# Kernel tuning notes

Hardware: AMD Instinct MI355X
Metric: run time of the kernel (lower is better)

## Reference

```python
import jax, jax.numpy as jnp
import numpy as np
from math import factorial, sqrt

L_MAX = 3
MUL = 64
# e3nn FullyConnectedTensorProduct instruction order: lexicographic over (l1, l2, l3)
# keeping paths with triangle inequality and matching parity ((-1)^(l1+l2) == (-1)^l3).
PATHS = [(l1, l2, l3)
         for l1 in range(L_MAX + 1)
         for l2 in range(L_MAX + 1)
         for l3 in range(L_MAX + 1)
         if abs(l1 - l2) <= l3 <= l1 + l2 and (l1 + l2 + l3) % 2 == 0]
assert len(PATHS) == 23
N_TO = {l3: sum(1 for p in PATHS if p[2] == l3) for l3 in range(L_MAX + 1)}


def _su2_cg(j1, m1, j2, m2, j3, m3):
    # Complex-basis Clebsch-Gordan coefficient (Racah formula), as in e3nn.
    if m3 != m1 + m2:
        return 0.0
    f = factorial
    vmin = max(-j1 + j2 + m3, -j1 + m1, 0)
    vmax = min(j2 + j3 + m1, j3 - j1 + j2, j3 + m3)
    c = sqrt((2 * j3 + 1) * f(j3 + j1 - j2) * f(j3 - j1 + j2) * f(j1 + j2 - j3)
             * f(j3 + m3) * f(j3 - m3)
             / (f(j1 + j2 + j3 + 1) * f(j1 - m1) * f(j1 + m1) * f(j2 - m2) * f(j2 + m2)))
    s = 0.0
    for v in range(vmin, vmax + 1):
        s += (-1) ** (v + j2 + m2) / f(v) * f(j2 + j3 + m1 - v) * f(j1 - m1 + v) \
             / f(j3 - j1 + j2 - v) / f(j3 + m3 - v) / f(v + j1 - j2 - m3)
    return c * s


def _q(l):
    # Change of basis real -> complex spherical harmonics (e3nn convention).
    q = np.zeros((2 * l + 1, 2 * l + 1), dtype=np.complex128)
    for m in range(-l, 0):
        q[l + m, l + abs(m)] = 1.0 / np.sqrt(2.0)
        q[l + m, l - abs(m)] = -1j / np.sqrt(2.0)
    q[l, l] = 1.0
    for m in range(1, l + 1):
        q[l + m, l + abs(m)] = (-1) ** m / np.sqrt(2.0)
        q[l + m, l - abs(m)] = 1j * (-1) ** m / np.sqrt(2.0)
    return (-1j) ** l * q


def _w3j(l1, l2, l3):
    # Real-basis Wigner 3j tensor, unit Frobenius norm (e3nn's o3.wigner_3j).
    csu2 = np.zeros((2 * l1 + 1, 2 * l2 + 1, 2 * l3 + 1))
    for m1 in range(-l1, l1 + 1):
        for m2 in range(-l2, l2 + 1):
            m3 = m1 + m2
            if -l3 <= m3 <= l3:
                csu2[l1 + m1, l2 + m2, l3 + m3] = _su2_cg(l1, m1, l2, m2, l3, m3)
    q1, q2, q3 = _q(l1), _q(l2), _q(l3)
    c = np.einsum('ij,kl,mn,ikn->jlm', q1, q2, np.conj(q3.T), csu2.astype(np.complex128))
    c = np.real(c)
    return (c / np.linalg.norm(c)).astype(np.float32)


W3J = {p: jnp.asarray(_w3j(*p)) for p in PATHS}
# e3nn 'component' irrep_normalization + 'element' path_normalization:
# per-path coeff = sqrt(ir_out.dim / (n_paths_into_out * mul1 * mul2)).
COEFF = {p: float(np.sqrt((2 * p[2] + 1) / (N_TO[p[2]] * MUL * MUL))) for p in PATHS}


def setup_inputs():
    key = jax.random.key(0)
    kx, kw = jax.random.split(key)
    x = jax.random.normal(kx, (2, 1024, MUL * (L_MAX + 1) ** 2), dtype=jnp.float32)
    weights = jax.random.normal(kw, (len(PATHS), MUL, MUL, MUL), dtype=jnp.float32)
    return {"x": x, "weights": weights}


def reference(x, weights):
    B, N, D = x.shape
    Z = B * N
    xf = x.reshape(Z, D)
    # e3nn layout: blocks of (mul, 2l+1) concatenated over l; offset = MUL * l^2.
    xs = [xf[:, MUL * l * l: MUL * (l + 1) ** 2].reshape(Z, MUL, 2 * l + 1)
          for l in range(L_MAX + 1)]
    acc = [jnp.zeros((Z, MUL, 2 * l + 1), dtype=x.dtype) for l in range(L_MAX + 1)]
    for p, (l1, l2, l3) in enumerate(PATHS):
        c = W3J[(l1, l2, l3)]
        t1 = jnp.einsum('zui,ijk->zujk', xs[l1], c)            # [Z,u,2l2+1,2l3+1]
        t2 = jnp.einsum('zujk,zvj->zuvk', t1, xs[l2])          # [Z,u,v,2l3+1]
        seg = jnp.einsum('zuvk,uvw->zwk', t2, weights[p]) * COEFF[(l1, l2, l3)]
        acc[l3] = acc[l3] + seg
    out = jnp.concatenate([a.reshape(Z, -1) for a in acc], axis=-1)
    return out.reshape(B, N, -1)
```

## Files before the change

kernel.cpp:

```cpp
#include <hip/hip_runtime.h>

struct CD { double re, im; };
constexpr CD cmul(CD a, CD b){ return CD{a.re*b.re - a.im*b.im, a.re*b.im + a.im*b.re}; }
constexpr CD conj_(CD a){ return CD{a.re, -a.im}; }

constexpr double factd(int n){ double r = 1.0; for(int i = 2; i <= n; ++i) r *= (double)i; return r; }
constexpr double csqrt_(double x){
  if (x <= 0.0) return 0.0;
  double g = x > 1.0 ? x : 1.0;
  for (int i = 0; i < 100; ++i) g = 0.5*(g + x/g);
  return g;
}

constexpr double su2_cg(int j1,int m1,int j2,int m2,int j3,int m3){
  if (m3 != m1 + m2) return 0.0;
  int vmin = -j1 + j2 + m3;
  if (-j1 + m1 > vmin) vmin = -j1 + m1;
  if (0 > vmin) vmin = 0;
  int vmax = j2 + j3 + m1;
  if (j3 - j1 + j2 < vmax) vmax = j3 - j1 + j2;
  if (j3 + m3 < vmax) vmax = j3 + m3;
  double c = csqrt_((2.0*j3 + 1.0) * factd(j3 + j1 - j2) * factd(j3 - j1 + j2) * factd(j1 + j2 - j3)
                    * factd(j3 + m3) * factd(j3 - m3)
                    / (factd(j1 + j2 + j3 + 1) * factd(j1 - m1) * factd(j1 + m1)
                       * factd(j2 - m2) * factd(j2 + m2)));
  double s = 0.0;
  for (int v = vmin; v <= vmax; ++v){
    double t = (((v + j2 + m2) & 1) ? -1.0 : 1.0) / factd(v)
               * factd(j2 + j3 + m1 - v) * factd(j1 - m1 + v)
               / factd(j3 - j1 + j2 - v) / factd(j3 + m3 - v) / factd(v + j1 - j2 - m3);
    s += t;
  }
  return c * s;
}

struct QM { CD m[7][7]; };
constexpr QM qmat(int l){
  QM q{};
  double is2 = 1.0 / csqrt_(2.0);
  for (int mm = -l; mm < 0; ++mm){
    q.m[l+mm][l-mm] = CD{is2, 0.0};
    q.m[l+mm][l+mm] = CD{0.0, -is2};
  }
  q.m[l][l] = CD{1.0, 0.0};
  for (int mm = 1; mm <= l; ++mm){
    double sgn = (mm & 1) ? -1.0 : 1.0;
    q.m[l+mm][l+mm] = CD{sgn*is2, 0.0};
    q.m[l+mm][l-mm] = CD{0.0, sgn*is2};
  }
  CD ph = (l % 4 == 0) ? CD{1,0} : (l % 4 == 1) ? CD{0,-1} : (l % 4 == 2) ? CD{-1,0} : CD{0,1};
  for (int r = 0; r < 7; ++r)
    for (int c = 0; c < 7; ++c)
      q.m[r][c] = cmul(ph, q.m[r][c]);
  return q;
}

template<int L1,int L2,int L3> struct W3JT { float v[2*L1+1][2*L2+1][2*L3+1]; };

template<int L1,int L2,int L3>
constexpr W3JT<L1,L2,L3> make_w3j(){
  constexpr int D1 = 2*L1+1, D2 = 2*L2+1, D3 = 2*L3+1;
  QM q1 = qmat(L1), q2 = qmat(L2), q3 = qmat(L3);
  double cg[7][7] = {};
  for (int i = 0; i < D1; ++i)
    for (int k = 0; k < D2; ++k){
      int n = i + k - L1 - L2 + L3;
      if (n >= 0 && n < D3) cg[i][k] = su2_cg(L1, i-L1, L2, k-L2, L3, (i-L1)+(k-L2));
    }
  double c[D1][D2][D3] = {};
  double norm2 = 0.0;
  for (int j = 0; j < D1; ++j)
    for (int l = 0; l < D2; ++l)
      for (int m = 0; m < D3; ++m){
        CD s{0.0, 0.0};
        for (int i = 0; i < D1; ++i)
          for (int k = 0; k < D2; ++k){
            double g = cg[i][k];
            if (g == 0.0) continue;
            int n = i + k - L1 - L2 + L3;
            CD t = cmul(q1.m[i][j], q2.m[k][l]);
            t = cmul(t, conj_(q3.m[n][m]));
            s.re += t.re * g; s.im += t.im * g;
          }
        c[j][l][m] = s.re;
        norm2 += s.re * s.re;
      }
  double inv = 1.0 / csqrt_(norm2);
  W3JT<L1,L2,L3> w{};
  for (int j = 0; j < D1; ++j)
    for (int l = 0; l < D2; ++l)
      for (int m = 0; m < D3; ++m){
        double val = c[j][l][m] * inv;
        if (val < 1e-10 && val > -1e-10) val = 0.0;
        w.v[j][l][m] = (float)val;
      }
  return w;
}

__device__ __constant__ int L3P_[23]  = {0,1,2,3,1,0,2,1,3,2,2,1,3,0,2,1,3,3,2,1,3,0,2};
__device__ __constant__ int SWAPP_[23] = {0,1,1,1,0,0,0,1,1,1,0,0,0,0,0,1,1,0,0,0,0,0,0};
constexpr int K3CUM[24] = {0,1,4,9,16,19,20,25,28,35,40,45,48,55,56,61,64,71,78,83,86,93,94,99};
constexpr size_t PSLICE = 2048ull * 64ull;

typedef __bf16 bf16x8 __attribute__((ext_vector_type(8)));
typedef float  f32x4  __attribute__((ext_vector_type(4)));
typedef float  f32x2  __attribute__((ext_vector_type(2)));

__global__ void pack_w_kernel(const float* __restrict__ w, unsigned short* __restrict__ wp, int total){
  int idx = blockIdx.x * 256 + threadIdx.x;
  if (idx >= total) return;
  int e    = idx & 7;
  int lane = (idx >> 3) & 63;
  int nt   = (idx >> 9) & 3;
  int hf   = (idx >> 11) & 1;
  int s    = (idx >> 12) & 63;
  int p    = idx >> 18;
  int kv = hf*32 + (lane >> 4)*8 + e;
  int wc = nt*16 + (lane & 15);
  int l3 = L3P_[p];
  const float nto[4] = {4.f, 6.f, 7.f, 6.f};
  float coeff = sqrtf((2.f*l3 + 1.f) / (nto[l3] * 4096.f));
  int a = SWAPP_[p] ? kv : s;
  int b = SWAPP_[p] ? s : kv;
  float val = w[(((size_t)p*64 + a)*64 + b)*64 + wc] * coeff;
  unsigned bits = __builtin_bit_cast(unsigned, val);
  unsigned r = (bits + 0x7FFFu + ((bits >> 16) & 1u)) >> 16;
  wp[idx] = (unsigned short)r;
}

__global__ void transpose_x(const float* __restrict__ x, float* __restrict__ xT){
  __shared__ float t[32][33];
  int bx = blockIdx.x, by = blockIdx.y;
  int tx = threadIdx.x & 31, ty = threadIdx.x >> 5;
  #pragma unroll
  for (int r = 0; r < 4; ++r)
    t[ty + r*8][tx] = x[(size_t)(by*32 + ty + r*8)*1024 + bx*32 + tx];
  __syncthreads();
  #pragma unroll
  for (int r = 0; r < 4; ++r)
    xT[(size_t)(bx*32 + ty + r*8)*2048 + by*32 + tx] = t[tx][ty + r*8];
}

template<int P,int L1,int L2,int L3,bool SWAP,int G0,int G,bool PART>
__device__ __forceinline__ void run_slot(
    int tile, const float* __restrict__ xT,
    const unsigned short* __restrict__ wp,
    float* __restrict__ dst, float* lds)
{
  constexpr int K3 = 2*L3+1;
  constexpr int LK = SWAP ? L1 : L2;
  constexpr int LS = SWAP ? L2 : L1;
  constexpr int DK = 2*LK+1, DS = 2*LS+1;
  constexpr auto C = make_w3j<L1,L2,L3>();

  const int lane = threadIdx.x & 63;
  const int wv   = threadIdx.x >> 6;
  const int zc   = tile*16 + (lane & 15);
  float* red = lds;
  float* tl  = lds + 3072 + wv*1040;

  f32x2 xk2[4][DK];
  {
    const float* xkb = xT + (size_t)(64*LK*LK)*2048 + zc;
    const int t0 = wv*32 + (lane >> 4)*8;
    #pragma unroll
    for (int q = 0; q < 4; ++q)
      #pragma unroll
      for (int t = 0; t < DK; ++t){
        float lo = xkb[(size_t)((t0 + 2*q    )*DK + t)*2048];
        float hi = xkb[(size_t)((t0 + 2*q + 1)*DK + t)*2048];
        xk2[q][t] = f32x2{lo, hi};
      }
  }

  const float* xsp = xT + (size_t)(64*LS*LS)*2048 + zc;
  const unsigned short* wu = wp + (size_t)P*262144 + (size_t)wv*2048 + (size_t)lane*8;

  f32x4 acc[G][4];
  #pragma unroll
  for (int a = 0; a < G; ++a)
    #pragma unroll
    for (int b = 0; b < 4; ++b) acc[a][b] = f32x4{0.f,0.f,0.f,0.f};

  float xs[DS];
  #pragma unroll
  for (int j = 0; j < DS; ++j) xs[j] = xsp[(size_t)j*2048];

  for (int s = 0; s < 64; ++s){
    bf16x8 bfrag[4];
    #pragma unroll
    for (int nt = 0; nt < 4; ++nt)
      bfrag[nt] = *reinterpret_cast<const bf16x8*>(wu + nt*512);

    const float* xnp = (s < 63) ? xsp + (size_t)DS*2048 : xsp;
    float xn[DS];
    #pragma unroll
    for (int j = 0; j < DS; ++j) xn[j] = xnp[(size_t)j*2048];

    #pragma unroll
    for (int kk = 0; kk < G; ++kk){
      float dk[DK];
      #pragma unroll
      for (int t = 0; t < DK; ++t) dk[t] = 0.f;
      #pragma unroll
      for (int t = 0; t < DK; ++t){
        #pragma unroll
        for (int j = 0; j < DS; ++j){
          const float cv = SWAP ? C.v[t][j][G0+kk] : C.v[j][t][G0+kk];
          if (cv != 0.0f) dk[t] = __builtin_fmaf(xs[j], cv, dk[t]);
        }
      }
      f32x2 af2[4];
      #pragma unroll
      for (int q = 0; q < 4; ++q) af2[q] = f32x2{0.f, 0.f};
      #pragma unroll
      for (int t = 0; t < DK; ++t){
        const f32x2 d2 = f32x2{dk[t], dk[t]};
        #pragma unroll
        for (int q = 0; q < 4; ++q)
          af2[q] += xk2[q][t] * d2;
      }
      bf16x8 af;
      #pragma unroll
      for (int q = 0; q < 4; ++q){
        af[2*q]   = (__bf16)af2[q].x;
        af[2*q+1] = (__bf16)af2[q].y;
      }
      __builtin_amdgcn_s_setprio(1);
      #pragma unroll
      for (int nt = 0; nt < 4; ++nt)
        acc[kk][nt] = __builtin_amdgcn_mfma_f32_16x16x32_bf16(af, bfrag[nt], acc[kk][nt], 0, 0, 0);
      __builtin_amdgcn_s_setprio(0);
    }
    #pragma unroll
    for (int j = 0; j < DS; ++j) xs[j] = xn[j];
    xsp += (size_t)DS*2048;
    wu  += 4096;
  }

  constexpr int Gh = (G + 1) / 2;
  static_assert(Gh <= 3, "red[] sized for Gh<=3");
  auto store_kk = [&](int kk, const f32x4 (&sum)[4]){
    if constexpr (PART){
      #pragma unroll
      for (int nt = 0; nt < 4; ++nt)
        #pragma unroll
        for (int r = 0; r < 4; ++r)
          tl[(((lane >> 4)*4 + r))*65 + nt*16 + (lane & 15)] = sum[nt][r];
      #pragma unroll
      for (int zr = 0; zr < 16; ++zr){
        float v = tl[zr*65 + lane];
        dst[(size_t)K3CUM[P]*PSLICE + ((size_t)(tile*16 + zr)*K3 + (G0+kk))*64 + lane] = v;
      }
    } else {
      #pragma unroll
      for (int nt = 0; nt < 4; ++nt)
        #pragma unroll
        for (int r = 0; r < 4; ++r){
          int zl = ((lane >> 4) << 2) + r;
          int wc = nt*16 + (lane & 15);
          unsafeAtomicAdd(dst + (size_t)(tile*16 + zl)*1024 + 64*L3*L3 + wc*K3 + (G0+kk),
                          sum[nt][r]);
        }
    }
  };

  if (wv == 1){
    #pragma unroll
    for (int kk = 0; kk < Gh; ++kk)
      #pragma unroll
      for (int nt = 0; nt < 4; ++nt)
        *reinterpret_cast<f32x4*>(&red[((kk*4 + nt)*64 + lane)*4]) = acc[kk][nt];
  }
  __syncthreads();
  if (wv == 0){
    #pragma unroll
    for (int kk = 0; kk < Gh; ++kk){
      f32x4 sum[4];
      #pragma unroll
      for (int nt = 0; nt < 4; ++nt){
        f32x4 o = *reinterpret_cast<const f32x4*>(&red[((kk*4 + nt)*64 + lane)*4]);
        sum[nt] = acc[kk][nt] + o;
      }
      store_kk(kk, sum);
    }
  }
  if constexpr (G > Gh){
    if (wv == 0){
      #pragma unroll
      for (int kk = Gh; kk < G; ++kk)
        #pragma unroll
        for (int nt = 0; nt < 4; ++nt)
          *reinterpret_cast<f32x4*>(&red[(((kk-Gh)*4 + nt)*64 + lane)*4]) = acc[kk][nt];
    }
    __syncthreads();
    if (wv == 1){
      #pragma unroll
      for (int kk = Gh; kk < G; ++kk){
        f32x4 sum[4];
        #pragma unroll
        for (int nt = 0; nt < 4; ++nt){
          f32x4 o = *reinterpret_cast<const f32x4*>(&red[(((kk-Gh)*4 + nt)*64 + lane)*4]);
          sum[nt] = acc[kk][nt] + o;
        }
        store_kk(kk, sum);
      }
    }
  }
}

template<bool PART>
__global__ __launch_bounds__(128, 3) void tp_main(const float* __restrict__ xT,
    const unsigned short* __restrict__ wp, float* __restrict__ dst)
{
  __shared__ __align__(16) float lds[5152];
  const int slot = blockIdx.x >> 7;
  const int tile = blockIdx.x & 127;
  switch (slot){
    case 0:  run_slot< 6,1,1,2,false,0,5,PART>(tile,xT,wp,dst,lds); break;
    case 1:  run_slot<16,2,3,3,true ,0,3,PART>(tile,xT,wp,dst,lds); break;
    case 2:  run_slot<20,3,2,3,false,0,3,PART>(tile,xT,wp,dst,lds); break;
    case 3:  run_slot<14,2,2,2,false,0,3,PART>(tile,xT,wp,dst,lds); break;
    case 4:  run_slot<15,2,3,1,true ,0,3,PART>(tile,xT,wp,dst,lds); break;
    case 5:  run_slot<19,3,2,1,false,0,3,PART>(tile,xT,wp,dst,lds); break;
    case 6:  run_slot< 8,1,2,3,true ,0,4,PART>(tile,xT,wp,dst,lds); break;
    case 7:  run_slot<12,2,1,3,false,0,4,PART>(tile,xT,wp,dst,lds); break;
    case 8:  run_slot<22,3,3,2,false,0,2,PART>(tile,xT,wp,dst,lds); break;
    case 9:  run_slot<22,3,3,2,false,2,2,PART>(tile,xT,wp,dst,lds); break;
    case 10: run_slot< 9,1,3,2,true ,0,3,PART>(tile,xT,wp,dst,lds); break;
    case 11: run_slot<16,2,3,3,true ,3,2,PART>(tile,xT,wp,dst,lds); break;
    case 12: run_slot<16,2,3,3,true ,5,2,PART>(tile,xT,wp,dst,lds); break;
    case 13: run_slot<20,3,2,3,false,3,2,PART>(tile,xT,wp,dst,lds); break;
    case 14: run_slot<20,3,2,3,false,5,2,PART>(tile,xT,wp,dst,lds); break;
    case 15: run_slot< 2,0,2,2,true ,0,5,PART>(tile,xT,wp,dst,lds); break;
    case 16: run_slot<10,2,0,2,false,0,5,PART>(tile,xT,wp,dst,lds); break;
    case 17: run_slot<11,2,1,1,false,0,3,PART>(tile,xT,wp,dst,lds); break;
    case 18: run_slot< 7,1,2,1,true ,0,3,PART>(tile,xT,wp,dst,lds); break;
    case 19: run_slot<18,3,1,2,false,0,3,PART>(tile,xT,wp,dst,lds); break;
    case 20: run_slot< 8,1,2,3,true ,4,3,PART>(tile,xT,wp,dst,lds); break;
    case 21: run_slot<12,2,1,3,false,4,3,PART>(tile,xT,wp,dst,lds); break;
    case 22: run_slot<14,2,2,2,false,3,2,PART>(tile,xT,wp,dst,lds); break;
    case 23: run_slot< 9,1,3,2,true ,3,2,PART>(tile,xT,wp,dst,lds); break;
    case 24: run_slot<18,3,1,2,false,3,2,PART>(tile,xT,wp,dst,lds); break;
    case 25: run_slot<22,3,3,2,false,4,1,PART>(tile,xT,wp,dst,lds); break;
    case 26: run_slot<21,3,3,0,false,0,1,PART>(tile,xT,wp,dst,lds); break;
    case 27: run_slot< 3,0,3,3,true ,0,4,PART>(tile,xT,wp,dst,lds); break;
    case 28: run_slot<17,3,0,3,false,0,4,PART>(tile,xT,wp,dst,lds); break;
    case 29: run_slot< 3,0,3,3,true ,4,3,PART>(tile,xT,wp,dst,lds); break;
    case 30: run_slot<17,3,0,3,false,4,3,PART>(tile,xT,wp,dst,lds); break;
    case 31: run_slot< 1,0,1,1,true ,0,3,PART>(tile,xT,wp,dst,lds); break;
    case 32: run_slot< 4,1,0,1,false,0,3,PART>(tile,xT,wp,dst,lds); break;
    case 33: run_slot<13,2,2,0,false,0,1,PART>(tile,xT,wp,dst,lds); break;
    case 34: run_slot< 5,1,1,0,false,0,1,PART>(tile,xT,wp,dst,lds); break;
    case 35: run_slot< 0,0,0,0,false,0,1,PART>(tile,xT,wp,dst,lds); break;
    default: break;
  }
}

__global__ void gather_out(const float* __restrict__ part, float* __restrict__ out){
  const int z = blockIdx.x;
  const int t = threadIdx.x;
  const int w = t & 63;
  const int g = t >> 6;
  float* ob = out + (size_t)z*1024;
  auto rd = [&](int p, int K3p, int k){
    return part[(size_t)K3CUM[p]*PSLICE + ((size_t)z*K3p + k)*64 + w];
  };
  if (g == 0){
    ob[w] = rd(0,1,0) + rd(5,1,0) + rd(13,1,0) + rd(21,1,0);
  } else if (g == 1){
    #pragma unroll
    for (int k = 0; k < 3; ++k)
      ob[64 + w*3 + k] = rd(1,3,k) + rd(4,3,k) + rd(7,3,k)
                       + rd(11,3,k) + rd(15,3,k) + rd(19,3,k);
  } else if (g == 2){
    #pragma unroll
    for (int k = 0; k < 5; ++k)
      ob[256 + w*5 + k] = rd(2,5,k) + rd(6,5,k) + rd(9,5,k) + rd(10,5,k)
                        + rd(14,5,k) + rd(18,5,k) + rd(22,5,k);
  } else {
    #pragma unroll
    for (int k = 0; k < 7; ++k)
      ob[576 + w*7 + k] = rd(3,7,k) + rd(8,7,k) + rd(12,7,k)
                        + rd(16,7,k) + rd(17,7,k) + rd(20,7,k);
  }
}

extern "C" void kernel_launch(void* const* d_in, const int* in_sizes, int n_in,
                              void* d_out, int out_size, void* d_ws, size_t ws_size,
                              hipStream_t stream)
{
  const float* x = (const float*)d_in[0];
  const float* w = (const float*)d_in[1];
  float* out = (float*)d_out;

  const size_t packB = 23ull*64*2*4*64*8 * sizeof(unsigned short);
  const size_t xTB   = 1024ull*2048*sizeof(float);
  const size_t partB = 99ull*PSLICE*sizeof(float);
  const int totalW = 23*64*2*4*64*8;

  unsigned short* wp = (unsigned short*)d_ws;
  float* xT   = (float*)((char*)d_ws + packB);
  float* part = (float*)((char*)d_ws + packB + xTB);

  if (ws_size < packB + xTB) return;

  pack_w_kernel<<<(totalW + 255)/256, 256, 0, stream>>>(w, wp, totalW);
  dim3 tg(32, 64);
  transpose_x<<<tg, 256, 0, stream>>>(x, xT);

  if (ws_size >= packB + xTB + partB){
    tp_main<true><<<36*128, 128, 0, stream>>>(xT, wp, part);
    gather_out<<<2048, 256, 0, stream>>>(part, out);
  } else {
    hipMemsetAsync(d_out, 0, (size_t)out_size * sizeof(float), stream);
    tp_main<false><<<36*128, 128, 0, stream>>>(xT, wp, out);
  }
}
```

Measured before the change: 199.1 us.

## Hoist W3J contraction out of inner loop by pre-contracting the fixed operand

Reorders the per-path contraction so the Wigner-3j coefficients are folded into the stationary operand once, before the 64-step loop. Each inner step then only does a single weighted sum over the streamed operand's components. This removes the per-iteration coefficient FMAs. The SWAP flags are inverted so the larger-l operand becomes the stationary one. In exchange the precomputed register array grows with G, which forces smaller k3 groups per block and raises the slot count from 36 to 46. That means more blocks, more re-reads of the streamed x and weights, and more register pressure.

```diff
diff --git a/kernel.cpp b/kernel.cpp
--- a/kernel.cpp
+++ b/kernel.cpp
@@ -98,7 +98,7 @@
 }
 
 __device__ __constant__ int L3P_[23]  = {0,1,2,3,1,0,2,1,3,2,2,1,3,0,2,1,3,3,2,1,3,0,2};
-__device__ __constant__ int SWAPP_[23] = {0,1,1,1,0,0,0,1,1,1,0,0,0,0,0,1,1,0,0,0,0,0,0};
+__device__ __constant__ int SWAPP_[23] = {1,0,0,0,1,1,1,0,0,0,1,1,1,1,1,0,0,1,1,1,1,1,1};
 constexpr int K3CUM[24] = {0,1,4,9,16,19,20,25,28,35,40,45,48,55,56,61,64,71,78,83,86,93,94,99};
 constexpr size_t PSLICE = 2048ull * 64ull;
 
@@ -159,18 +159,36 @@
   float* red = lds;
   float* tl  = lds + 3072 + wv*1040;
 
-  f32x2 xk2[4][DK];
+  f32x2 yk[G][4][DS];
+  #pragma unroll
+  for (int kk = 0; kk < G; ++kk)
+    #pragma unroll
+    for (int q = 0; q < 4; ++q)
+      #pragma unroll
+      for (int j = 0; j < DS; ++j) yk[kk][q][j] = f32x2{0.f, 0.f};
   {
     const float* xkb = xT + (size_t)(64*LK*LK)*2048 + zc;
     const int t0 = wv*32 + (lane >> 4)*8;
     #pragma unroll
-    for (int q = 0; q < 4; ++q)
-      #pragma unroll
-      for (int t = 0; t < DK; ++t){
-        float lo = xkb[(size_t)((t0 + 2*q    )*DK + t)*2048];
-        float hi = xkb[(size_t)((t0 + 2*q + 1)*DK + t)*2048];
-        xk2[q][t] = f32x2{lo, hi};
-      }
+    for (int t = 0; t < DK; ++t){
+      f32x2 xt[4];
+      #pragma unroll
+      for (int q = 0; q < 4; ++q)
+        xt[q] = f32x2{ xkb[(size_t)((t0 + 2*q    )*DK + t)*2048],
+                       xkb[(size_t)((t0 + 2*q + 1)*DK + t)*2048] };
+      #pragma unroll
+      for (int kk = 0; kk < G; ++kk)
+        #pragma unroll
+        for (int j = 0; j < DS; ++j){
+          const float cv = SWAP ? C.v[t][j][G0+kk] : C.v[j][t][G0+kk];
+          if (cv != 0.0f){
+            const f32x2 c2 = f32x2{cv, cv};
+            #pragma unroll
+            for (int q = 0; q < 4; ++q)
+              yk[kk][q][j] += xt[q] * c2;
+          }
+        }
+    }
   }
 
   const float* xsp = xT + (size_t)(64*LS*LS)*2048 + zc;
@@ -199,26 +217,15 @@
 
     #pragma unroll
     for (int kk = 0; kk < G; ++kk){
-      float dk[DK];
-      #pragma unroll
-      for (int t = 0; t < DK; ++t) dk[t] = 0.f;
-      #pragma unroll
-      for (int t = 0; t < DK; ++t){
-        #pragma unroll
-        for (int j = 0; j < DS; ++j){
-          const float cv = SWAP ? C.v[t][j][G0+kk] : C.v[j][t][G0+kk];
-          if (cv != 0.0f) dk[t] = __builtin_fmaf(xs[j], cv, dk[t]);
-        }
-      }
       f32x2 af2[4];
       #pragma unroll
       for (int q = 0; q < 4; ++q) af2[q] = f32x2{0.f, 0.f};
       #pragma unroll
-      for (int t = 0; t < DK; ++t){
-        const f32x2 d2 = f32x2{dk[t], dk[t]};
+      for (int j = 0; j < DS; ++j){
+        const f32x2 d2 = f32x2{xs[j], xs[j]};
         #pragma unroll
         for (int q = 0; q < 4; ++q)
-          af2[q] += xk2[q][t] * d2;
+          af2[q] += yk[kk][q][j] * d2;
       }
       bf16x8 af;
       #pragma unroll
@@ -317,42 +324,52 @@
   const int slot = blockIdx.x >> 7;
   const int tile = blockIdx.x & 127;
   switch (slot){
-    case 0:  run_slot< 6,1,1,2,false,0,5,PART>(tile,xT,wp,dst,lds); break;
-    case 1:  run_slot<16,2,3,3,true ,0,3,PART>(tile,xT,wp,dst,lds); break;
-    case 2:  run_slot<20,3,2,3,false,0,3,PART>(tile,xT,wp,dst,lds); break;
-    case 3:  run_slot<14,2,2,2,false,0,3,PART>(tile,xT,wp,dst,lds); break;
-    case 4:  run_slot<15,2,3,1,true ,0,3,PART>(tile,xT,wp,dst,lds); break;
-    case 5:  run_slot<19,3,2,1,false,0,3,PART>(tile,xT,wp,dst,lds); break;
-    case 6:  run_slot< 8,1,2,3,true ,0,4,PART>(tile,xT,wp,dst,lds); break;
-    case 7:  run_slot<12,2,1,3,false,0,4,PART>(tile,xT,wp,dst,lds); break;
-    case 8:  run_slot<22,3,3,2,false,0,2,PART>(tile,xT,wp,dst,lds); break;
-    case 9:  run_slot<22,3,3,2,false,2,2,PART>(tile,xT,wp,dst,lds); break;
-    case 10: run_slot< 9,1,3,2,true ,0,3,PART>(tile,xT,wp,dst,lds); break;
-    case 11: run_slot<16,2,3,3,true ,3,2,PART>(tile,xT,wp,dst,lds); break;
-    case 12: run_slot<16,2,3,3,true ,5,2,PART>(tile,xT,wp,dst,lds); break;
-    case 13: run_slot<20,3,2,3,false,3,2,PART>(tile,xT,wp,dst,lds); break;
-    case 14: run_slot<20,3,2,3,false,5,2,PART>(tile,xT,wp,dst,lds); break;
-    case 15: run_slot< 2,0,2,2,true ,0,5,PART>(tile,xT,wp,dst,lds); break;
-    case 16: run_slot<10,2,0,2,false,0,5,PART>(tile,xT,wp,dst,lds); break;
-    case 17: run_slot<11,2,1,1,false,0,3,PART>(tile,xT,wp,dst,lds); break;
-    case 18: run_slot< 7,1,2,1,true ,0,3,PART>(tile,xT,wp,dst,lds); break;
-    case 19: run_slot<18,3,1,2,false,0,3,PART>(tile,xT,wp,dst,lds); break;
-    case 20: run_slot< 8,1,2,3,true ,4,3,PART>(tile,xT,wp,dst,lds); break;
-    case 21: run_slot<12,2,1,3,false,4,3,PART>(tile,xT,wp,dst,lds); break;
-    case 22: run_slot<14,2,2,2,false,3,2,PART>(tile,xT,wp,dst,lds); break;
-    case 23: run_slot< 9,1,3,2,true ,3,2,PART>(tile,xT,wp,dst,lds); break;
-    case 24: run_slot<18,3,1,2,false,3,2,PART>(tile,xT,wp,dst,lds); break;
-    case 25: run_slot<22,3,3,2,false,4,1,PART>(tile,xT,wp,dst,lds); break;
-    case 26: run_slot<21,3,3,0,false,0,1,PART>(tile,xT,wp,dst,lds); break;
-    case 27: run_slot< 3,0,3,3,true ,0,4,PART>(tile,xT,wp,dst,lds); break;
-    case 28: run_slot<17,3,0,3,false,0,4,PART>(tile,xT,wp,dst,lds); break;
-    case 29: run_slot< 3,0,3,3,true ,4,3,PART>(tile,xT,wp,dst,lds); break;
-    case 30: run_slot<17,3,0,3,false,4,3,PART>(tile,xT,wp,dst,lds); break;
-    case 31: run_slot< 1,0,1,1,true ,0,3,PART>(tile,xT,wp,dst,lds); break;
-    case 32: run_slot< 4,1,0,1,false,0,3,PART>(tile,xT,wp,dst,lds); break;
-    case 33: run_slot<13,2,2,0,false,0,1,PART>(tile,xT,wp,dst,lds); break;
-    case 34: run_slot< 5,1,1,0,false,0,1,PART>(tile,xT,wp,dst,lds); break;
-    case 35: run_slot< 0,0,0,0,false,0,1,PART>(tile,xT,wp,dst,lds); break;
+    case 0:  run_slot<22,3,3,2,true ,0,1,PART>(tile,xT,wp,dst,lds); break;
+    case 1:  run_slot<22,3,3,2,true ,1,1,PART>(tile,xT,wp,dst,lds); break;
+    case 2:  run_slot<22,3,3,2,true ,2,1,PART>(tile,xT,wp,dst,lds); break;
+    case 3:  run_slot<22,3,3,2,true ,3,1,PART>(tile,xT,wp,dst,lds); break;
+    case 4:  run_slot<22,3,3,2,true ,4,1,PART>(tile,xT,wp,dst,lds); break;
+    case 5:  run_slot<16,2,3,3,false,0,2,PART>(tile,xT,wp,dst,lds); break;
+    case 6:  run_slot<16,2,3,3,false,2,2,PART>(tile,xT,wp,dst,lds); break;
+    case 7:  run_slot<16,2,3,3,false,4,2,PART>(tile,xT,wp,dst,lds); break;
+    case 8:  run_slot<16,2,3,3,false,6,1,PART>(tile,xT,wp,dst,lds); break;
+    case 9:  run_slot<20,3,2,3,true ,0,2,PART>(tile,xT,wp,dst,lds); break;
+    case 10: run_slot<20,3,2,3,true ,2,2,PART>(tile,xT,wp,dst,lds); break;
+    case 11: run_slot<20,3,2,3,true ,4,2,PART>(tile,xT,wp,dst,lds); break;
+    case 12: run_slot<20,3,2,3,true ,6,1,PART>(tile,xT,wp,dst,lds); break;
+    case 13: run_slot<14,2,2,2,true ,0,2,PART>(tile,xT,wp,dst,lds); break;
+    case 14: run_slot<14,2,2,2,true ,2,2,PART>(tile,xT,wp,dst,lds); break;
+    case 15: run_slot<14,2,2,2,true ,4,1,PART>(tile,xT,wp,dst,lds); break;
+    case 16: run_slot<21,3,3,0,true ,0,1,PART>(tile,xT,wp,dst,lds); break;
+    case 17: run_slot<15,2,3,1,false,0,2,PART>(tile,xT,wp,dst,lds); break;
+    case 18: run_slot<15,2,3,1,false,2,1,PART>(tile,xT,wp,dst,lds); break;
+    case 19: run_slot<19,3,2,1,true ,0,2,PART>(tile,xT,wp,dst,lds); break;
+    case 20: run_slot<19,3,2,1,true ,2,1,PART>(tile,xT,wp,dst,lds); break;
+    case 21: run_slot<13,2,2,0,true ,0,1,PART>(tile,xT,wp,dst,lds); break;
+    case 22: run_slot< 8,1,2,3,false,0,3,PART>(tile,xT,wp,dst,lds); break;
+    case 23: run_slot< 8,1,2,3,false,3,3,PART>(tile,xT,wp,dst,lds); break;
+    case 24: run_slot< 8,1,2,3,false,6,1,PART>(tile,xT,wp,dst,lds); break;
+    case 25: run_slot<12,2,1,3,true ,0,3,PART>(tile,xT,wp,dst,lds); break;
+    case 26: run_slot<12,2,1,3,true ,3,3,PART>(tile,xT,wp,dst,lds); break;
+    case 27: run_slot<12,2,1,3,true ,6,1,PART>(tile,xT,wp,dst,lds); break;
+    case 28: run_slot< 6,1,1,2,true ,0,3,PART>(tile,xT,wp,dst,lds); break;
+    case 29: run_slot< 6,1,1,2,true ,3,2,PART>(tile,xT,wp,dst,lds); break;
+    case 30: run_slot< 9,1,3,2,false,0,3,PART>(tile,xT,wp,dst,lds); break;
+    case 31: run_slot< 9,1,3,2,false,3,2,PART>(tile,xT,wp,dst,lds); break;
+    case 32: run_slot<18,3,1,2,true ,0,3,PART>(tile,xT,wp,dst,lds); break;
+    case 33: run_slot<18,3,1,2,true ,3,2,PART>(tile,xT,wp,dst,lds); break;
+    case 34: run_slot< 7,1,2,1,false,0,3,PART>(tile,xT,wp,dst,lds); break;
+    case 35: run_slot<11,2,1,1,true ,0,3,PART>(tile,xT,wp,dst,lds); break;
+    case 36: run_slot< 5,1,1,0,true ,0,1,PART>(tile,xT,wp,dst,lds); break;
+    case 37: run_slot< 3,0,3,3,false,0,5,PART>(tile,xT,wp,dst,lds); break;
+    case 38: run_slot< 3,0,3,3,false,5,2,PART>(tile,xT,wp,dst,lds); break;
+    case 39: run_slot<17,3,0,3,true ,0,5,PART>(tile,xT,wp,dst,lds); break;
+    case 40: run_slot<17,3,0,3,true ,5,2,PART>(tile,xT,wp,dst,lds); break;
+    case 41: run_slot< 2,0,2,2,false,0,5,PART>(tile,xT,wp,dst,lds); break;
+    case 42: run_slot<10,2,0,2,true ,0,5,PART>(tile,xT,wp,dst,lds); break;
+    case 43: run_slot< 1,0,1,1,false,0,3,PART>(tile,xT,wp,dst,lds); break;
+    case 44: run_slot< 4,1,0,1,true ,0,3,PART>(tile,xT,wp,dst,lds); break;
+    case 45: run_slot< 0,0,0,0,true ,0,1,PART>(tile,xT,wp,dst,lds); break;
     default: break;
   }
 }
@@ -410,10 +427,10 @@
   transpose_x<<<tg, 256, 0, stream>>>(x, xT);
 
   if (ws_size >= packB + xTB + partB){
-    tp_main<true><<<36*128, 128, 0, stream>>>(xT, wp, part);
+    tp_main<true><<<46*128, 128, 0, stream>>>(xT, wp, part);
     gather_out<<<2048, 256, 0, stream>>>(part, out);
   } else {
     hipMemsetAsync(d_out, 0, (size_t)out_size * sizeof(float), stream);
-    tp_main<false><<<36*128, 128, 0, stream>>>(xT, wp, out);
-  }
-}
+    tp_main<false><<<46*128, 128, 0, stream>>>(xT, wp, out);
+  }
+}
```

New measurement: 211.3 us. 6.1% more time.
